# Optimization experiments

Hardware: AMD Instinct MI355X
Metric: run time of the kernel (lower is better)

The kernel has to match this reference:

```python
import jax, jax.numpy as jnp
import numpy as np
from jax import lax

E = 8          # num_experts
K = 2          # top-k
TASKS = 8
GATE_DIM = 16
# (in, expand, out, kernel, stride) per MoE stage
STAGES = [(3, 32, 16, 7, 2), (16, 64, 32, 3, 1), (32, 128, 64, 3, 2), (64, 256, 64, 3, 1), (64, 128, 32, 3, 1)]
DN = ('NCHW', 'OIHW', 'NCHW')


def _pw(x, w):
    return lax.conv_general_dilated(x, w, (1, 1), 'VALID', dimension_numbers=DN)


def _dw(x, w, s):
    p = w.shape[-1] // 2
    return lax.conv_general_dilated(x, w, (s, s), [(p, p), (p, p)], dimension_numbers=DN, feature_group_count=x.shape[1])


def _gn(x, scale, bias):
    # GroupNorm with num_groups = C // 4, eps = 1e-5 (torch default)
    B, C, H, W = x.shape
    G = C // 4
    xr = x.reshape(B, G, -1)
    m = xr.mean(-1, keepdims=True)
    v = xr.var(-1, keepdims=True)
    xn = ((xr - m) * lax.rsqrt(v + 1e-5)).reshape(B, C, H, W)
    return xn * scale[None, :, None, None] + bias[None, :, None, None]


def _dsc(x, p, stride):
    # DSCBlock: pw-conv -> GN -> SiLU -> dw-conv -> GN -> SiLU -> pw-conv -> GN
    w1, s1, b1, w2, s2, b2, w3, s3, b3 = p
    x = jax.nn.silu(_gn(_pw(x, w1), s1, b1))
    x = jax.nn.silu(_gn(_dw(x, w2, stride), s2, b2))
    return _gn(_pw(x, w3), s3, b3)


def _moe(gate_input, x, wg, p, stride, task_bh):
    # task-conditioned top-k softmax gating (noisy_gating=False, all aux loss weights 0)
    logits = gate_input @ wg[task_bh]                      # (B, E)
    probs = jax.nn.softmax(logits, axis=-1)
    topv, topi = lax.top_k(probs, K)
    topv = topv / topv.sum(-1, keepdims=True)              # renormalize top-k gates
    Bn = gate_input.shape[0]
    dense = jnp.zeros_like(probs).at[jnp.arange(Bn)[:, None], topi].set(topv)
    eo = jax.vmap(lambda pe: _dsc(x, pe, stride))(p)       # (E, B, C, H, W)
    return jnp.einsum('be,ebchw->bchw', dense, eo)


def _forward(fl, task_bh):
    gi, xi, ppe = fl[0], fl[1], fl[2]
    x = xi
    for i, (_, _, _, _, s) in enumerate(STAGES):
        base = 3 + i * 10
        wg = fl[base]
        p = tuple(fl[base + 1: base + 10])
        x = _moe(gi, x, wg, p, s, task_bh)
    Bn = x.shape[0]
    # patchify: (B,32,20,20) -> unfold(2,4,4).unfold(3,4,4) -> permute -> (B,25,512)
    patches = x.reshape(Bn, 32, 5, 4, 5, 4).transpose(0, 1, 2, 4, 3, 5)  # (B,32,5,5,4,4)
    patches = patches.transpose(0, 2, 3, 4, 5, 1).reshape(Bn, 25, 512)
    return patches + ppe


def setup_inputs():
    key = jax.random.key(0)
    ks = iter(jax.random.split(key, 256))
    B = 64
    d = {}
    d['gate_input'] = jax.random.normal(next(ks), (B, GATE_DIM), jnp.float32)
    d['expert_input'] = jax.random.normal(next(ks), (B, 3, 80, 80), jnp.float32)
    d['patch_pos_embed'] = 0.02 * jax.random.normal(next(ks), (1, 25, 512), jnp.float32)
    for i, (cin, exp, cout, k, s) in enumerate(STAGES, 1):
        d[f's{i}_wg'] = 0.1 * jax.random.normal(next(ks), (TASKS, GATE_DIM, E), jnp.float32)
        d[f's{i}_w1'] = jax.random.normal(next(ks), (E, exp, cin, 1, 1), jnp.float32) / np.sqrt(cin)
        d[f's{i}_g1s'] = 1.0 + 0.1 * jax.random.normal(next(ks), (E, exp), jnp.float32)
        d[f's{i}_g1b'] = 0.1 * jax.random.normal(next(ks), (E, exp), jnp.float32)
        d[f's{i}_w2'] = jax.random.normal(next(ks), (E, exp, 1, k, k), jnp.float32) / k
        d[f's{i}_g2s'] = 1.0 + 0.1 * jax.random.normal(next(ks), (E, exp), jnp.float32)
        d[f's{i}_g2b'] = 0.1 * jax.random.normal(next(ks), (E, exp), jnp.float32)
        d[f's{i}_w3'] = jax.random.normal(next(ks), (E, cout, exp, 1, 1), jnp.float32) / np.sqrt(exp)
        d[f's{i}_g3s'] = 1.0 + 0.1 * jax.random.normal(next(ks), (E, cout), jnp.float32)
        d[f's{i}_g3b'] = 0.1 * jax.random.normal(next(ks), (E, cout), jnp.float32)
    d['task_bh'] = 3
    return d


def reference(gate_input, expert_input, patch_pos_embed, s1_wg, s1_w1, s1_g1s, s1_g1b, s1_w2, s1_g2s, s1_g2b, s1_w3, s1_g3s, s1_g3b, s2_wg, s2_w1, s2_g1s, s2_g1b, s2_w2, s2_g2s, s2_g2b, s2_w3, s2_g3s, s2_g3b, s3_wg, s3_w1, s3_g1s, s3_g1b, s3_w2, s3_g2s, s3_g2b, s3_w3, s3_g3s, s3_g3b, s4_wg, s4_w1, s4_g1s, s4_g1b, s4_w2, s4_g2s, s4_g2b, s4_w3, s4_g3s, s4_g3b, s5_wg, s5_w1, s5_g1s, s5_g1b, s5_w2, s5_g2s, s5_g2b, s5_w3, s5_g3s, s5_g3b, task_bh):
    fl = (gate_input, expert_input, patch_pos_embed,
          s1_wg, s1_w1, s1_g1s, s1_g1b, s1_w2, s1_g2s, s1_g2b, s1_w3, s1_g3s, s1_g3b,
          s2_wg, s2_w1, s2_g1s, s2_g1b, s2_w2, s2_g2s, s2_g2b, s2_w3, s2_g3s, s2_g3b,
          s3_wg, s3_w1, s3_g1s, s3_g1b, s3_w2, s3_g2s, s3_g2b, s3_w3, s3_g3s, s3_g3b,
          s4_wg, s4_w1, s4_g1s, s4_g1b, s4_w2, s4_g2s, s4_g2b, s4_w3, s4_g3s, s4_g3b,
          s5_wg, s5_w1, s5_g1s, s5_g1b, s5_w2, s5_g2s, s5_g2b, s5_w3, s5_g3s, s5_g3b)
    patches = _forward(fl, task_bh)
    loss = jnp.zeros((), patches.dtype)  # all MoE loss weights are 0 in VisionEncoder
    return (patches, loss)
```

## Files before the change

### kernel.cpp

```cpp
#include <hip/hip_runtime.h>
#include <cstddef>

#define TPB 256

typedef __attribute__((ext_vector_type(8))) short short8v;
typedef __attribute__((ext_vector_type(4))) float f32x4;

__device__ __forceinline__ int rfl(int v) { return __builtin_amdgcn_readfirstlane(v); }
__device__ __forceinline__ float rflf(float v) {
    return __int_as_float(__builtin_amdgcn_readfirstlane(__float_as_int(v)));
}

__device__ __forceinline__ unsigned short f2bf(float f) {
    union { float f; unsigned int u; } x{f};
    unsigned int r = x.u + 0x7fffu + ((x.u >> 16) & 1u);
    return (unsigned short)(r >> 16);
}
__device__ __forceinline__ float bf2f(unsigned short u) {
    return __uint_as_float(((unsigned int)u) << 16);
}

template <int N, int NW>
__device__ __forceinline__ void bredN(float* v, float* red) {
    __syncthreads();
// ... 35 lines not shown
    const int task = taskp[0];
    const float* wg = gp.wg[s] + (size_t)task * 16 * 8;
    float l[8];
    #pragma unroll
    for (int e = 0; e < 8; e++) l[e] = 0.f;
    for (int d = 0; d < 16; d++) {
        float v = gi[b * 16 + d];
        #pragma unroll
        for (int e = 0; e < 8; e++) l[e] += v * wg[d * 8 + e];
    }
    float mx = l[0];
    #pragma unroll
    for (int e = 1; e < 8; e++) mx = fmaxf(mx, l[e]);
    float p[8]; float sum = 0.f;
    #pragma unroll
    for (int e = 0; e < 8; e++) { p[e] = expf(l[e] - mx); sum += p[e]; }
    int i0 = 0;
    #pragma unroll
    for (int e = 1; e < 8; e++) if (p[e] > p[i0]) i0 = e;
    int i1 = (i0 == 0) ? 1 : 0;
    #pragma unroll
    for (int e = 0; e < 8; e++) if (e != i0 && p[e] > p[i1]) i1 = e;
    const float denom = p[i0] + p[i1];
    const int base = (s * 64 + b) * 2;
    gidx[base] = i0; gidx[base + 1] = i1;
    gw[base] = p[i0] / denom; gw[base + 1] = p[i1] / denom;
}

template <int M, int K, int N, int MT, int NCHK, bool FOLD, bool BIN>
__global__ __launch_bounds__(256) void gemm_bf16(
    const unsigned short* __restrict__ inp, const float* __restrict__ wmat,
    const int* __restrict__ gidx, const float* __restrict__ foldStats,
    const float* __restrict__ foldS, const float* __restrict__ foldB,
    unsigned short* __restrict__ outp, float* __restrict__ stats) {
    constexpr int KITERS = (K + 31) / 32;
    constexpr int IM = (MT == 64) ? 2 : 1;
    constexpr int IN = (MT == 16) ? 1 : 2;
    const int bx = blockIdx.x;
    const int nc = bx % NCHK, mc = bx / NCHK;
    const int b = blockIdx.y, slot = blockIdx.z;
    const int bs = b * 2 + slot;
    const int e = rfl(gidx[b * 2 + slot]);
    const int n0 = nc * 64, m0 = mc * MT;
    const int tid = threadIdx.x;
    const int lane = tid & 63, wv = tid >> 6;
    const int quad = lane >> 4, l15 = lane & 15;

    __shared__ __align__(16) unsigned short wtile[MT * 40];
    __shared__ unsigned int intile[16 * 65];
    __shared__ float sred[(MT / 4) * 2];
    __shared__ float afv[K], bfv[K];

    if (tid < (MT / 4) * 2) sred[tid] = 0.f;
    if constexpr (FOLD) {
        for (int c = tid; c < K; c += 256) {
            const int g = c >> 2;
            const float s1 = foldStats[((size_t)bs * (K / 4) + g) * 2 + 0];
            const float s2 = foldStats[((size_t)bs * (K / 4) + g) * 2 + 1];
            const float mean = s1 / (4.f * N);
            const float var = s2 / (4.f * N) - mean * mean;
            const float inv = rsqrtf(var + 1e-5f);
            const float sc = foldS[e * K + c], bi = foldB[e * K + c];
            afv[c] = inv * sc;
            bfv[c] = bi - mean * inv * sc;
        }
    }

    int mbase, nbase;
    if constexpr (MT == 64) { mbase = (wv & 1) * 32; nbase = (wv >> 1) * 32; }
    else if constexpr (MT == 32) { mbase = (wv & 1) * 16; nbase = (wv >> 1) * 32; }
    else { mbase = 0; nbase = wv * 16; }

    f32x4 acc[IM][IN];
    #pragma unroll
    for (int im = 0; im < IM; im++)
        #pragma unroll
        for (int in = 0; in < IN; in++)
            #pragma unroll
            for (int r = 0; r < 4; r++) acc[im][in][r] = 0.f;

    const unsigned short* ib = inp + (size_t)(BIN ? b : bs) * K * N;
    const float* wbase = wmat + (size_t)e * M * K;

    for (int k0 = 0; k0 < KITERS * 32; k0 += 32) {
        __syncthreads();
        for (int i = tid; i < MT * 32; i += 256) {
            const int m = i >> 5, kk = i & 31;
            const float v = (k0 + kk < K) ? wbase[(size_t)(m0 + m) * K + k0 + kk] : 0.f;
            wtile[m * 40 + kk] = f2bf(v);
        }
        {
            const int kp = tid >> 4, nq = tid & 15;
            const int k = k0 + kp * 2;
            const int n = n0 + nq * 4;
            unsigned short u0[4] = {0, 0, 0, 0}, u1[4] = {0, 0, 0, 0};
            const bool nv = (n < N);
            if (nv && k < K) {
                const ushort4 t = *(const ushort4*)(ib + (size_t)k * N + n);
                u0[0] = t.x; u0[1] = t.y; u0[2] = t.z; u0[3] = t.w;
            }
            if (nv && k + 1 < K) {
                const ushort4 t = *(const ushort4*)(ib + (size_t)(k + 1) * N + n);
                u1[0] = t.x; u1[1] = t.y; u1[2] = t.z; u1[3] = t.w;
            }
            #pragma unroll
            for (int t = 0; t < 4; t++) {
                float f0, f1;
                if constexpr (FOLD) {
                    f0 = (nv && k < K) ? silu_f(afv[k] * bf2f(u0[t]) + bfv[k]) : 0.f;
                    f1 = (nv && k + 1 < K) ? silu_f(afv[k + 1] * bf2f(u1[t]) + bfv[k + 1]) : 0.f;
                } else {
                    f0 = bf2f(u0[t]); f1 = bf2f(u1[t]);
                }
                intile[kp * 65 + nq * 4 + t] =
                    (unsigned int)f2bf(f0) | ((unsigned int)f2bf(f1) << 16);
            }
        }
        __syncthreads();

        short8v afr[IM];
        #pragma unroll
        for (int im = 0; im < IM; im++) {
            const int m = mbase + im * 16 + l15;
            afr[im] = *(const short8v*)&wtile[m * 40 + quad * 8];
        }
        #pragma unroll
        for (int in = 0; in < IN; in++) {
            union { unsigned int u[4]; short8v s; } bu;
            const int col = nbase + in * 16 + l15;
            #pragma unroll
            for (int i = 0; i < 4; i++) bu.u[i] = intile[(quad * 4 + i) * 65 + col];
            #pragma unroll
            for (int im = 0; im < IM; im++)
                acc[im][in] = __builtin_amdgcn_mfma_f32_16x16x32_bf16(
                    afr[im], bu.s, acc[im][in], 0, 0, 0);
        }
    }

    unsigned short* ob = outp + (size_t)bs * M * N;
    #pragma unroll
    for (int im = 0; im < IM; im++) {
        #pragma unroll
        for (int in = 0; in < IN; in++) {
            const int n = n0 + nbase + in * 16 + l15;
            float s1 = 0.f, s2 = 0.f;
            #pragma unroll
            for (int r = 0; r < 4; r++) {
                const float a = acc[im][in][r];
                s1 += a; s2 += a * a;
            }
            if (n < N) {
                #pragma unroll
                for (int r = 0; r < 4; r++) {
                    const int m = m0 + mbase + im * 16 + quad * 4 + r;
                    ob[(size_t)m * N + n] = f2bf(acc[im][in][r]);
                }
            }
            #pragma unroll
            for (int off = 8; off > 0; off >>= 1) {
                s1 += __shfl_down(s1, off, 16);
                s2 += __shfl_down(s2, off, 16);
            }
            if (l15 == 0) {
                const int gl = (mbase + im * 16) / 4 + quad;
                atomicAdd(&sred[gl * 2 + 0], s1);
                atomicAdd(&sred[gl * 2 + 1], s2);
            }
        }
    }
    __syncthreads();
    for (int i = tid; i < MT / 4; i += 256) {
        float* sp = stats + (((size_t)bs * (M / 4) + mc * (MT / 4) + i) * NCHK + nc) * 2;
        sp[0] = sred[i * 2]; sp[1] = sred[i * 2 + 1];
    }
}

template <int CEXP, int H, int W, int NCH, int TPBk, int NCHK1>
__global__ __launch_bounds__(TPBk) void dw_k(
    const unsigned short* __restrict__ raw1, const float* __restrict__ stats1,
    const float* __restrict__ g1s, const float* __restrict__ g1b,
    const float* __restrict__ w2, const int* __restrict__ gidx,
    unsigned short* __restrict__ act2raw, float* __restrict__ stats2) {
    constexpr int HW = H * W, HP = H + 2, WPL = W + 3;
    constexpr int NPV = HW / 4, NG = NCH / 4, NW = TPBk / 64;
    constexpr int Qc = HW / 4, QT = NCH * Qc, QI = (QT + TPBk - 1) / TPBk;
    constexpr int G1 = CEXP / 4;
    const int gch = blockIdx.x, b = blockIdx.y, slot = blockIdx.z;
    const int bs = b * 2 + slot;
    const int tid = threadIdx.x;
    const int e = rfl(gidx[b * 2 + slot]);
    const int cb0 = gch * NCH;

    __shared__ float buf1[NCH * HP * WPL];
    __shared__ float w2s[NCH * 9];
    __shared__ float afl[NCH], bfl[NCH];
    __shared__ float red[2 * NG * NW];

    for (int i = tid; i < NCH * HP * WPL; i += TPBk) buf1[i] = 0.f;
    if (tid < NCH * 9) w2s[tid] = w2[((size_t)e * CEXP + cb0) * 9 + tid];
    if (tid < NCH) {
        const int c = cb0 + tid, g = c >> 2;
        float s1 = 0.f, s2 = 0.f;
        for (int i = 0; i < NCHK1; i++) {
            s1 += stats1[(((size_t)bs * G1 + g) * NCHK1 + i) * 2 + 0];
            s2 += stats1[(((size_t)bs * G1 + g) * NCHK1 + i) * 2 + 1];
        }
        const float mean = s1 / (4.f * HW);
        const float var = s2 / (4.f * HW) - mean * mean;
        const float inv = rsqrtf(var + 1e-5f);
        const float sc = g1s[e * CEXP + c], bi = g1b[e * CEXP + c];
        afl[tid] = inv * sc; bfl[tid] = bi - mean * inv * sc;
    }
    __syncthreads();

    const unsigned short* rb = raw1 + (size_t)bs * CEXP * HW + (size_t)cb0 * HW;
    for (int i = tid; i < NCH * NPV; i += TPBk) {
        const int c = i / NPV, pv = i - c * NPV;
        const int p4 = pv * 4, ph = p4 / W, pwb = p4 - ph * W;
        const ushort4 u = *(const ushort4*)(rb + (size_t)c * HW + p4);
        const float a = afl[c], bb = bfl[c];
        float* bp = &buf1[(c * HP + ph + 1) * WPL + pwb + 1];
        bp[0] = silu_f(a * bf2f(u.x) + bb);
        bp[1] = silu_f(a * bf2f(u.y) + bb);
        bp[2] = silu_f(a * bf2f(u.z) + bb);
        bp[3] = silu_f(a * bf2f(u.w) + bb);
    }
    __syncthreads();

    float st2[2 * NG];
    #pragma unroll
    for (int i = 0; i < 2 * NG; i++) st2[i] = 0.f;
    unsigned short* ao = act2raw + (size_t)bs * CEXP * HW + (size_t)cb0 * HW;
    #pragma unroll
    for (int qi = 0; qi < QI; qi++) {
        const int q = tid + qi * TPBk;
        if (QI * TPBk == QT || q < QT) {
            const int c = q / Qc, qq = q - c * Qc;
            const int oh = qq % H, owb = (qq / H) * 4;
            float o[4] = {0.f, 0.f, 0.f, 0.f};
            #pragma unroll
            for (int kh = 0; kh < 3; kh++) {
                const int base = (c * HP + oh + kh) * WPL + owb;
                float r[6];
                #pragma unroll
                for (int i = 0; i < 6; i++) r[i] = buf1[base + i];
                const float wa = w2s[c * 9 + kh * 3 + 0];
                const float wb = w2s[c * 9 + kh * 3 + 1];
                const float wcc = w2s[c * 9 + kh * 3 + 2];
                #pragma unroll
                for (int t = 0; t < 4; t++)
                    o[t] += wa * r[t] + wb * r[t + 1] + wcc * r[t + 2];
            }
            ushort4 ov = {f2bf(o[0]), f2bf(o[1]), f2bf(o[2]), f2bf(o[3])};
            *(ushort4*)(ao + c * HW + oh * W + owb) = ov;
            #pragma unroll
            for (int t = 0; t < 4; t++) {
                if constexpr (NG == 1) { st2[0] += o[t]; st2[1] += o[t] * o[t]; }
                else {
                    const bool gs = (c >= 4);
                    float a0 = gs ? 0.f : o[t], a1 = gs ? o[t] : 0.f;
                    st2[0] += a0; st2[1] += a0 * a0;
                    st2[2] += a1; st2[3] += a1 * a1;
                }
            }
        }
    }
    bredN<2 * NG, NW>(st2, red);
    if (tid == 0) {
        #pragma unroll
        for (int g = 0; g < NG; g++) {
            stats2[((size_t)bs * G1 + cb0 / 4 + g) * 2 + 0] = st2[g * 2];
            stats2[((size_t)bs * G1 + cb0 / 4 + g) * 2 + 1] = st2[g * 2 + 1];
        }
    }
}

__global__ __launch_bounds__(256) void s1_stats(
    const float* __restrict__ xin, const float* __restrict__ w1,
    const int* __restrict__ gidx, float* __restrict__ stats1) {
    const int g = blockIdx.x, b = blockIdx.y, slot = blockIdx.z;
    const int tid = threadIdx.x;
    const int e = rfl(gidx[b * 2 + slot]);
    __shared__ float red[8];
    const float* xb = xin + (size_t)b * 3 * 6400;
    const float* w1e = w1 + ((size_t)e * 32 + g * 4) * 3;
    float wr[4][3];
    #pragma unroll
    for (int c = 0; c < 4; c++)
        #pragma unroll
        for (int k = 0; k < 3; k++) wr[c][k] = rflf(w1e[c * 3 + k]);
    float s[2] = {0.f, 0.f};
    #pragma unroll
    for (int j = 0; j < 7; j++) {
        const int i = j * 256 + tid;
        if (i < 1600) {
            const int p4 = i * 4;
            const float4 v0 = *(const float4*)(xb + p4);
            const float4 v1 = *(const float4*)(xb + 6400 + p4);
            const float4 v2 = *(const float4*)(xb + 12800 + p4);
            const float a0[4] = {v0.x, v0.y, v0.z, v0.w};
            const float a1[4] = {v1.x, v1.y, v1.z, v1.w};
            const float a2[4] = {v2.x, v2.y, v2.z, v2.w};
            #pragma unroll
            for (int t = 0; t < 4; t++)
                #pragma unroll
// ... 130 lines not shown
    const float* __restrict__ g2s, const float* __restrict__ g2b,
    const int* __restrict__ gidx, unsigned short* __restrict__ act2) {
    const int g = blockIdx.x, b = blockIdx.y, slot = blockIdx.z;
    const int tid = threadIdx.x;
    const int e = rfl(gidx[b * 2 + slot]);
    const float* sp = stats2 + ((size_t)(b * 2 + slot) * 8 + g) * 8;
    const float s1 = rflf(sp[0]) + rflf(sp[2]) + rflf(sp[4]) + rflf(sp[6]);
    const float s2 = rflf(sp[1]) + rflf(sp[3]) + rflf(sp[5]) + rflf(sp[7]);
    const float mean2 = s1 / 6400.f;
    const float var2 = s2 / 6400.f - mean2 * mean2;
    const float inv2 = rsqrtf(var2 + 1e-5f);
    const float* rb = rawdw + (size_t)(b * 2 + slot) * 32 * 1600 + (size_t)g * 4 * 1600;
    unsigned short* ao = act2 + ((size_t)(b * 2 + slot) * 32 + g * 4) * 1600;
    #pragma unroll
    for (int c = 0; c < 4; c++) {
        const float sc = rflf(g2s[e * 32 + g * 4 + c]);
        const float bi = rflf(g2b[e * 32 + g * 4 + c]);
        #pragma unroll
        for (int qi = 0; qi < 2; qi++) {
            const int i = tid + qi * 256;
            if (i < 400) {
                const float4 v = *(const float4*)(rb + c * 1600 + i * 4);
                ushort4 ov;
                ov.x = f2bf(silu_f((v.x - mean2) * inv2 * sc + bi));
                ov.y = f2bf(silu_f((v.y - mean2) * inv2 * sc + bi));
                ov.z = f2bf(silu_f((v.z - mean2) * inv2 * sc + bi));
                ov.w = f2bf(silu_f((v.w - mean2) * inv2 * sc + bi));
                *(ushort4*)(ao + c * 1600 + i * 4) = ov;
            }
        }
    }
}

template <int CIN, int CEXP, int KS, int STRIDE, int H, int W, int HO, int WO,
          int NCH, int TPBk>
__global__ __launch_bounds__(TPBk) void dsc_ab_v2(
    const unsigned short* __restrict__ xin, const float* __restrict__ w1,
    const float* __restrict__ g1s, const float* __restrict__ g1b,
    const float* __restrict__ w2,
    const float* __restrict__ g2s, const float* __restrict__ g2b,
    const int* __restrict__ gidx, unsigned short* __restrict__ act2) {
    constexpr int HW = H * W, HWO = HO * WO;
    constexpr int HP = H + 2, WPL = W + 3, EVW = (W + 2) / 2;
    constexpr int NPV = HW / 4;
    constexpr int JN = (NPV + TPBk - 1) / TPBk;
    constexpr int NW = TPBk / 64;
    constexpr int NG = NCH / 4;
    constexpr int Qc = HWO / 4;
    constexpr int QT = NCH * Qc;
    constexpr int QI = (QT + TPBk - 1) / TPBk;
    constexpr int KK = KS * KS;
    const int gch = blockIdx.x, b = blockIdx.y, slot = blockIdx.z;
    const int tid = threadIdx.x;
    const int e = rfl(gidx[b * 2 + slot]);
    const int cb0 = gch * NCH;

    __shared__ float buf1[NCH * HP * WPL];
    __shared__ float w2s[NCH * KK];
    __shared__ float sc2s[NCH], bi2s[NCH];
    __shared__ float red[2 * NG * NW];

    for (int i = tid; i < NCH * HP * WPL; i += TPBk) buf1[i] = 0.f;
    for (int i = tid; i < NCH * KK; i += TPBk) {
        int c = i / KK, k = i - c * KK;
        w2s[i] = w2[((size_t)e * CEXP + cb0 + c) * KK + k];
    }
    if (tid < NCH) {
        sc2s[tid] = g2s[e * CEXP + cb0 + tid];
        bi2s[tid] = g2b[e * CEXP + cb0 + tid];
    }

    const unsigned short* xb = xin + (size_t)b * CIN * HW;
    const float* w1e = w1 + ((size_t)e * CEXP + cb0) * CIN;

    float acc[NCH][JN][4];
    #pragma unroll
    for (int c = 0; c < NCH; c++)
        #pragma unroll
        for (int j = 0; j < JN; j++)
            #pragma unroll
            for (int t = 0; t < 4; t++) acc[c][j][t] = 0.f;

    for (int cb = 0; cb < CIN; cb += 4) {
        float wr[NCH][4];
        #pragma unroll
        for (int c = 0; c < NCH; c++)
            #pragma unroll
            for (int k = 0; k < 4; k++) wr[c][k] = rflf(w1e[c * CIN + cb + k]);
        #pragma unroll
        for (int j = 0; j < JN; j++) {
            const int pv = tid + j * TPBk;
            if (JN * TPBk == NPV || pv < NPV) {
                #pragma unroll
                for (int k = 0; k < 4; k++) {
                    const ushort4 v4 = *(const ushort4*)(xb + (cb + k) * HW + pv * 4);
                    const float va[4] = {bf2f(v4.x), bf2f(v4.y), bf2f(v4.z), bf2f(v4.w)};
                    #pragma unroll
                    for (int c = 0; c < NCH; c++)
                        #pragma unroll
                        for (int t = 0; t < 4; t++)
                            acc[c][j][t] = fmaf(wr[c][k], va[t], acc[c][j][t]);
                }
            }
        }
    }
    float st[2 * NG];
    #pragma unroll
    for (int i = 0; i < 2 * NG; i++) st[i] = 0.f;
    #pragma unroll
    for (int c = 0; c < NCH; c++) {
        const int gs = (c >> 2) * 2;
        #pragma unroll
        for (int j = 0; j < JN; j++)
            #pragma unroll
            for (int t = 0; t < 4; t++) {
                float a = acc[c][j][t];
                st[gs] += a; st[gs + 1] += a * a;
            }
    }
    bredN<2 * NG, NW>(st, red);
    float mg[NG], ig[NG];
    #pragma unroll
    for (int g = 0; g < NG; g++) {
        mg[g] = st[g * 2] / (4.f * HW);
        float var = st[g * 2 + 1] / (4.f * HW) - mg[g] * mg[g];
        ig[g] = rsqrtf(var + 1e-5f);
    }
    float sc1r[NCH], bi1r[NCH];
    #pragma unroll
    for (int c = 0; c < NCH; c++) {
        sc1r[c] = rflf(g1s[e * CEXP + cb0 + c]);
        bi1r[c] = rflf(g1b[e * CEXP + cb0 + c]);
    }
    #pragma unroll
    for (int j = 0; j < JN; j++) {
        const int pv = tid + j * TPBk;
        if (JN * TPBk == NPV || pv < NPV) {
            const int p4 = pv * 4;
            const int ph = p4 / W, pwb = p4 - ph * W;
            #pragma unroll
            for (int c = 0; c < NCH; c++) {
                const int g = (NG == 1) ? 0 : (c >> 2);
                #pragma unroll
                for (int t = 0; t < 4; t++) {
                    float v = silu_f((acc[c][j][t] - mg[g]) * ig[g] * sc1r[c] + bi1r[c]);
                    const int j2 = pwb + t + 1;
                    const int col = (STRIDE == 1) ? j2
                                    : ((j2 & 1) ? EVW + (j2 >> 1) : (j2 >> 1));
                    buf1[(c * HP + ph + 1) * WPL + col] = v;
                }
            }
        }
    }
    __syncthreads();

    float dacc[QI][4];
    float st2[2 * NG];
    #pragma unroll
    for (int i = 0; i < 2 * NG; i++) st2[i] = 0.f;
    #pragma unroll
    for (int qi = 0; qi < QI; qi++) {
        #pragma unroll
        for (int t = 0; t < 4; t++) dacc[qi][t] = 0.f;
        const int q = tid + qi * TPBk;
        if (QI * TPBk == QT || q < QT) {
            const int c = q / Qc, qq = q - c * Qc;
            const int oh = qq % HO, owb = (qq / HO) * 4;
            float o[4] = {0.f, 0.f, 0.f, 0.f};
            if (STRIDE == 1) {
                #pragma unroll
                for (int kh = 0; kh < KS; kh++) {
                    const int base = (c * HP + oh + kh) * WPL + owb;
                    float r[6];
                    #pragma unroll
                    for (int i = 0; i < 6; i++) r[i] = buf1[base + i];
                    const float wa = w2s[c * KK + kh * KS + 0];
                    const float wb = w2s[c * KK + kh * KS + 1];
                    const float wcc = w2s[c * KK + kh * KS + 2];
                    #pragma unroll
                    for (int t = 0; t < 4; t++)
                        o[t] += wa * r[t] + wb * r[t + 1] + wcc * r[t + 2];
                }
            } else {
                #pragma unroll
                for (int kh = 0; kh < KS; kh++) {
                    const int base = (c * HP + 2 * oh + kh) * WPL;
                    float ev[5], od[4];
                    #pragma unroll
                    for (int i = 0; i < 5; i++) ev[i] = buf1[base + owb + i];
                    #pragma unroll
                    for (int i = 0; i < 4; i++) od[i] = buf1[base + EVW + owb + i];
                    const float wa = w2s[c * KK + kh * KS + 0];
                    const float wb = w2s[c * KK + kh * KS + 1];
                    const float wcc = w2s[c * KK + kh * KS + 2];
                    #pragma unroll
                    for (int t = 0; t < 4; t++)
                        o[t] += wa * ev[t] + wb * od[t] + wcc * ev[t + 1];
                }
            }
            #pragma unroll
            for (int t = 0; t < 4; t++) {
                float a = o[t];
                dacc[qi][t] = a;
                if constexpr (NG == 1) {
                    st2[0] += a; st2[1] += a * a;
                } else {
                    const bool gsel = (c >= 4);
                    float a0 = gsel ? 0.f : a, a1 = gsel ? a : 0.f;
                    st2[0] += a0; st2[1] += a0 * a0;
                    st2[2] += a1; st2[3] += a1 * a1;
                }
            }
        }
    }
    bredN<2 * NG, NW>(st2, red);
    float m2[NG], i2[NG];
    #pragma unroll
    for (int g = 0; g < NG; g++) {
        m2[g] = st2[g * 2] / (4.f * HWO);
        float var = st2[g * 2 + 1] / (4.f * HWO) - m2[g] * m2[g];
        i2[g] = rsqrtf(var + 1e-5f);
    }
    unsigned short* ao = act2 + ((size_t)(b * 2 + slot) * CEXP + cb0) * HWO;
    #pragma unroll
    for (int qi = 0; qi < QI; qi++) {
        const int q = tid + qi * TPBk;
        if (QI * TPBk == QT || q < QT) {
            const int c = q / Qc, qq = q - c * Qc;
            const int oh = qq % HO, owb = (qq / HO) * 4;
            const int g = (NG == 1) ? 0 : ((c >= 4) ? 1 : 0);
            const float sc = sc2s[c], bi = bi2s[c];
            ushort4 ov;
            ov.x = f2bf(silu_f((dacc[qi][0] - m2[g]) * i2[g] * sc + bi));
            ov.y = f2bf(silu_f((dacc[qi][1] - m2[g]) * i2[g] * sc + bi));
            ov.z = f2bf(silu_f((dacc[qi][2] - m2[g]) * i2[g] * sc + bi));
            ov.w = f2bf(silu_f((dacc[qi][3] - m2[g]) * i2[g] * sc + bi));
            *(ushort4*)(ao + c * HWO + oh * WO + owb) = ov;
        }
    }
}

template <int COUT, int HWO, int PXC, bool PATCH>
__global__ __launch_bounds__(256) void pw3_k3m(
    const unsigned short* __restrict__ raw3, const float* __restrict__ statsw,
    const float* __restrict__ g3s, const float* __restrict__ g3b,
    const int* __restrict__ gidx, const float* __restrict__ gw,
    const float* __restrict__ ppe, float* __restrict__ outf,
    unsigned short* __restrict__ outb) {
    constexpr int G = COUT / 4;
    constexpr int Q = HWO / 4;
    const int gg = blockIdx.x, b = blockIdx.y;
    const int tid = threadIdx.x;

    float A[2][4], Bv[2][4];
    #pragma unroll
    for (int slot = 0; slot < 2; slot++) {
        const int e = rfl(gidx[b * 2 + slot]);
        const float wgt = rflf(gw[b * 2 + slot]);
        const float* sp = statsw + ((size_t)(b * 2 + slot) * G + gg) * PXC * 2;
        float s1 = 0.f, s2 = 0.f;
        for (int i = 0; i < PXC; i++) { s1 += rflf(sp[i * 2]); s2 += rflf(sp[i * 2 + 1]); }
        const float mean = s1 / (4.f * HWO);
        const float var = s2 / (4.f * HWO) - mean * mean;
        const float inv = rsqrtf(var + 1e-5f);
        #pragma unroll
        for (int i = 0; i < 4; i++) {
            const int c = gg * 4 + i;
            const float sc = rflf(g3s[e * COUT + c]);
            const float bi = rflf(g3b[e * COUT + c]);
            A[slot][i] = wgt * inv * sc;
            Bv[slot][i] = wgt * (bi - mean * inv * sc);
        }
    }

// ... 23 lines not shown
                const float* pp = ppe + p * 512;
                #pragma unroll
                for (int jj = 0; jj < 4; jj++)
                    op[dbase + jj * 32] = o[jj] + pp[dbase + jj * 32];
            }
        }
    }
    if (PATCH && gg == 0 && b == 0 && tid == 0) outf[64 * 25 * 512] = 0.f;
}

extern "C" void kernel_launch(void* const* d_in, const int* in_sizes, int n_in,
                              void* d_out, int out_size, void* d_ws, size_t ws_size,
                              hipStream_t stream) {
    const float* gate_input = (const float*)d_in[0];
    const float* expert_input = (const float*)d_in[1];
    const float* ppe = (const float*)d_in[2];
    const int* taskp = (const int*)d_in[53];
    auto in = [&](int s, int k) { return (const float*)d_in[3 + s * 10 + k]; };

    char* ws = (char*)d_ws;
    int* gidx = (int*)ws;
    float* gw = (float*)(ws + 4096);
    size_t off = 8192;
    unsigned short* x0 = (unsigned short*)(ws + off); off += (size_t)8 << 20;
    unsigned short* x1 = (unsigned short*)(ws + off); off += (size_t)8 << 20;
    unsigned short* act2 = (unsigned short*)(ws + off); off += (size_t)27 << 20;
    char* bufA = ws + off; off += (size_t)27 << 20;
    float* stats1 = (float*)(ws + off); off += (size_t)2 << 20;
    float* stats2 = (float*)(ws + off); off += 262144;
    float* stats3 = (float*)(ws + off); off += (size_t)1 << 20;
    float* st1a = (float*)(ws + off); off += 65536;
    float* st1b = (float*)(ws + off);
    float* outp = (float*)d_out;

    GatePtrs gp;
    for (int s = 0; s < 5; s++) gp.wg[s] = in(s, 0);
    gate_kernel<<<5, 64, 0, stream>>>(gate_input, gp, taskp, gidx, gw);

    s1_stats<<<dim3(8, 64, 2), 256, 0, stream>>>(expert_input, in(0, 1),
                                                 gidx + 0 * 128, st1a);
    s1_band<<<dim3(32, 64, 2), 256, 0, stream>>>(
        expert_input, in(0, 1), in(0, 2), in(0, 3), in(0, 4),
        gidx + 0 * 128, st1a, (float*)bufA, st1b);
    s1_norm<<<dim3(8, 64, 2), 256, 0, stream>>>(
        (float*)bufA, st1b, in(0, 5), in(0, 6), gidx + 0 * 128, act2);
    gemm_bf16<16, 32, 1600, 16, 25, false, false><<<dim3(25, 64, 2), 256, 0, stream>>>(
        act2, in(0, 7), gidx + 0 * 128, nullptr, nullptr, nullptr,
        (unsigned short*)bufA, stats3);
    pw3_k3m<16, 1600, 25, false><<<dim3(4, 64), 256, 0, stream>>>(
        (unsigned short*)bufA, stats3, in(0, 8), in(0, 9), gidx + 0 * 128,
        gw + 0 * 128, ppe, nullptr, x0);

    gemm_bf16<64, 16, 1600, 64, 25, false, true><<<dim3(25, 64, 2), 256, 0, stream>>>(
        x0, in(1, 1), gidx + 1 * 128, nullptr, nullptr, nullptr,
        (unsigned short*)bufA, stats1);
    dw_k<64, 40, 40, 4, 256, 25><<<dim3(16, 64, 2), 256, 0, stream>>>(
        (unsigned short*)bufA, stats1, in(1, 2), in(1, 3), in(1, 4),
        gidx + 1 * 128, act2, stats2);
    gemm_bf16<32, 64, 1600, 32, 25, true, false><<<dim3(25, 64, 2), 256, 0, stream>>>(
        act2, in(1, 7), gidx + 1 * 128, stats2, in(1, 5), in(1, 6),
        (unsigned short*)bufA, stats3);
    pw3_k3m<32, 1600, 25, false><<<dim3(8, 64), 256, 0, stream>>>(
        (unsigned short*)bufA, stats3, in(1, 8), in(1, 9), gidx + 1 * 128,
        gw + 1 * 128, ppe, nullptr, x1);

    dsc_ab_v2<32, 128, 3, 2, 40, 40, 20, 20, 4, 256><<<dim3(32, 64, 2), 256, 0, stream>>>(
        x1, in(2, 1), in(2, 2), in(2, 3), in(2, 4), in(2, 5), in(2, 6),
        gidx + 2 * 128, act2);
    gemm_bf16<64, 128, 400, 64, 7, false, false><<<dim3(7, 64, 2), 256, 0, stream>>>(
        act2, in(2, 7), gidx + 2 * 128, nullptr, nullptr, nullptr,
        (unsigned short*)bufA, stats3);
    pw3_k3m<64, 400, 7, false><<<dim3(16, 64), 256, 0, stream>>>(
        (unsigned short*)bufA, stats3, in(2, 8), in(2, 9), gidx + 2 * 128,
        gw + 2 * 128, ppe, nullptr, x0);

    gemm_bf16<256, 64, 400, 64, 7, false, true><<<dim3(28, 64, 2), 256, 0, stream>>>(
        x0, in(3, 1), gidx + 3 * 128, nullptr, nullptr, nullptr,
        (unsigned short*)bufA, stats1);
    dw_k<256, 20, 20, 8, 128, 7><<<dim3(32, 64, 2), 128, 0, stream>>>(
        (unsigned short*)bufA, stats1, in(3, 2), in(3, 3), in(3, 4),
        gidx + 3 * 128, act2, stats2);
    gemm_bf16<64, 256, 400, 64, 7, true, false><<<dim3(7, 64, 2), 256, 0, stream>>>(
        act2, in(3, 7), gidx + 3 * 128, stats2, in(3, 5), in(3, 6),
        (unsigned short*)bufA, stats3);
    pw3_k3m<64, 400, 7, false><<<dim3(16, 64), 256, 0, stream>>>(
        (unsigned short*)bufA, stats3, in(3, 8), in(3, 9), gidx + 3 * 128,
        gw + 3 * 128, ppe, nullptr, x1);

    gemm_bf16<128, 64, 400, 64, 7, false, true><<<dim3(14, 64, 2), 256, 0, stream>>>(
        x1, in(4, 1), gidx + 4 * 128, nullptr, nullptr, nullptr,
        (unsigned short*)bufA, stats1);
    dw_k<128, 20, 20, 8, 128, 7><<<dim3(16, 64, 2), 128, 0, stream>>>(
        (unsigned short*)bufA, stats1, in(4, 2), in(4, 3), in(4, 4),
        gidx + 4 * 128, act2, stats2);
    gemm_bf16<32, 128, 400, 32, 7, true, false><<<dim3(7, 64, 2), 256, 0, stream>>>(
        act2, in(4, 7), gidx + 4 * 128, stats2, in(4, 5), in(4, 6),
        (unsigned short*)bufA, stats3);
    pw3_k3m<32, 400, 7, true><<<dim3(8, 64), 256, 0, stream>>>(
        (unsigned short*)bufA, stats3, in(4, 8), in(4, 9), gidx + 4 * 128,
        gw + 4 * 128, ppe, outp, nullptr);
}
```

Measured before the change: 523.9 us.

## Split bf16 weights into hi/lo MFMA passes and replace stage-3 fused dsc kernel

Every pointwise GEMM now splits each fp32 weight into a high and a low bf16 part and issues two MFMAs per tile, which doubles matrix work and LDS traffic for weights in exchange for near-fp32 weight precision. The stage-3 fused pointwise+depthwise kernel is removed. It is replaced by two GEMM halves over 64 channels each, followed by a strided depthwise kernel, and the final GEMM now folds the GroupNorm. The dw kernel gains stride and channel-offset support. This looks mainly like an accuracy fix that adds launches and compute.

```diff
diff --git a/kernel.cpp b/kernel.cpp
--- a/kernel.cpp
+++ b/kernel.cpp
@@ -91,7 +91,8 @@
     const unsigned short* __restrict__ inp, const float* __restrict__ wmat,
     const int* __restrict__ gidx, const float* __restrict__ foldStats,
     const float* __restrict__ foldS, const float* __restrict__ foldB,
-    unsigned short* __restrict__ outp, float* __restrict__ stats) {
+    unsigned short* __restrict__ outp, float* __restrict__ stats,
+    int mfull, int moff) {
     constexpr int KITERS = (K + 31) / 32;
     constexpr int IM = (MT == 64) ? 2 : 1;
     constexpr int IN = (MT == 16) ? 1 : 2;
@@ -105,7 +106,8 @@
     const int lane = tid & 63, wv = tid >> 6;
     const int quad = lane >> 4, l15 = lane & 15;
 
-    __shared__ __align__(16) unsigned short wtile[MT * 40];
+    __shared__ __align__(16) unsigned short wtileH[MT * 40];
+    __shared__ __align__(16) unsigned short wtileL[MT * 40];
     __shared__ unsigned int intile[16 * 65];
     __shared__ float sred[(MT / 4) * 2];
     __shared__ float afv[K], bfv[K];
@@ -139,14 +141,16 @@
             for (int r = 0; r < 4; r++) acc[im][in][r] = 0.f;
 
     const unsigned short* ib = inp + (size_t)(BIN ? b : bs) * K * N;
-    const float* wbase = wmat + (size_t)e * M * K;
+    const float* wbase = wmat + ((size_t)e * mfull + moff) * K;
 
     for (int k0 = 0; k0 < KITERS * 32; k0 += 32) {
         __syncthreads();
         for (int i = tid; i < MT * 32; i += 256) {
             const int m = i >> 5, kk = i & 31;
             const float v = (k0 + kk < K) ? wbase[(size_t)(m0 + m) * K + k0 + kk] : 0.f;
-            wtile[m * 40 + kk] = f2bf(v);
+            const unsigned short h = f2bf(v);
+            wtileH[m * 40 + kk] = h;
+            wtileL[m * 40 + kk] = f2bf(v - bf2f(h));
         }
         {
             const int kp = tid >> 4, nq = tid & 15;
@@ -177,11 +181,12 @@
         }
         __syncthreads();
 
-        short8v afr[IM];
+        short8v afrH[IM], afrL[IM];
         #pragma unroll
         for (int im = 0; im < IM; im++) {
             const int m = mbase + im * 16 + l15;
-            afr[im] = *(const short8v*)&wtile[m * 40 + quad * 8];
+            afrH[im] = *(const short8v*)&wtileH[m * 40 + quad * 8];
+            afrL[im] = *(const short8v*)&wtileL[m * 40 + quad * 8];
         }
         #pragma unroll
         for (int in = 0; in < IN; in++) {
@@ -190,9 +195,12 @@
             #pragma unroll
             for (int i = 0; i < 4; i++) bu.u[i] = intile[(quad * 4 + i) * 65 + col];
             #pragma unroll
-            for (int im = 0; im < IM; im++)
+            for (int im = 0; im < IM; im++) {
                 acc[im][in] = __builtin_amdgcn_mfma_f32_16x16x32_bf16(
-                    afr[im], bu.s, acc[im][in], 0, 0, 0);
+                    afrH[im], bu.s, acc[im][in], 0, 0, 0);
+                acc[im][in] = __builtin_amdgcn_mfma_f32_16x16x32_bf16(
+                    afrL[im], bu.s, acc[im][in], 0, 0, 0);
+            }
         }
     }
 
@@ -229,26 +237,29 @@
     }
     __syncthreads();
     for (int i = tid; i < MT / 4; i += 256) {
-        float* sp = stats + (((size_t)bs * (M / 4) + mc * (MT / 4) + i) * NCHK + nc) * 2;
+        float* sp = stats + (((size_t)bs * (mfull / 4) + moff / 4 + mc * (MT / 4) + i)
+                             * NCHK + nc) * 2;
         sp[0] = sred[i * 2]; sp[1] = sred[i * 2 + 1];
     }
 }
 
-template <int CEXP, int H, int W, int NCH, int TPBk, int NCHK1>
+template <int CLOC, int CFULL, int H, int W, int STRIDE, int NCH, int TPBk, int NCHK1>
 __global__ __launch_bounds__(TPBk) void dw_k(
     const unsigned short* __restrict__ raw1, const float* __restrict__ stats1,
     const float* __restrict__ g1s, const float* __restrict__ g1b,
     const float* __restrict__ w2, const int* __restrict__ gidx,
-    unsigned short* __restrict__ act2raw, float* __restrict__ stats2) {
+    unsigned short* __restrict__ act2raw, float* __restrict__ stats2, int coff) {
     constexpr int HW = H * W, HP = H + 2, WPL = W + 3;
+    constexpr int HO = H / STRIDE, WO = W / STRIDE, HWO = HO * WO;
     constexpr int NPV = HW / 4, NG = NCH / 4, NW = TPBk / 64;
-    constexpr int Qc = HW / 4, QT = NCH * Qc, QI = (QT + TPBk - 1) / TPBk;
-    constexpr int G1 = CEXP / 4;
+    constexpr int Qc = HWO / 4, QT = NCH * Qc, QI = (QT + TPBk - 1) / TPBk;
+    constexpr int G1 = CFULL / 4;
     const int gch = blockIdx.x, b = blockIdx.y, slot = blockIdx.z;
     const int bs = b * 2 + slot;
     const int tid = threadIdx.x;
     const int e = rfl(gidx[b * 2 + slot]);
     const int cb0 = gch * NCH;
+    const int cg0 = coff + cb0;
 
     __shared__ float buf1[NCH * HP * WPL];
     __shared__ float w2s[NCH * 9];
@@ -256,9 +267,9 @@
     __shared__ float red[2 * NG * NW];
 
     for (int i = tid; i < NCH * HP * WPL; i += TPBk) buf1[i] = 0.f;
-    if (tid < NCH * 9) w2s[tid] = w2[((size_t)e * CEXP + cb0) * 9 + tid];
+    if (tid < NCH * 9) w2s[tid] = w2[((size_t)e * CFULL + cg0) * 9 + tid];
     if (tid < NCH) {
-        const int c = cb0 + tid, g = c >> 2;
+        const int g = (cg0 + tid) >> 2;
         float s1 = 0.f, s2 = 0.f;
         for (int i = 0; i < NCHK1; i++) {
             s1 += stats1[(((size_t)bs * G1 + g) * NCHK1 + i) * 2 + 0];
@@ -267,12 +278,12 @@
         const float mean = s1 / (4.f * HW);
         const float var = s2 / (4.f * HW) - mean * mean;
         const float inv = rsqrtf(var + 1e-5f);
-        const float sc = g1s[e * CEXP + c], bi = g1b[e * CEXP + c];
+        const float sc = g1s[e * CFULL + cg0 + tid], bi = g1b[e * CFULL + cg0 + tid];
         afl[tid] = inv * sc; bfl[tid] = bi - mean * inv * sc;
     }
     __syncthreads();
 
-    const unsigned short* rb = raw1 + (size_t)bs * CEXP * HW + (size_t)cb0 * HW;
+    const unsigned short* rb = raw1 + (size_t)bs * CLOC * HW + (size_t)cb0 * HW;
     for (int i = tid; i < NCH * NPV; i += TPBk) {
         const int c = i / NPV, pv = i - c * NPV;
         const int p4 = pv * 4, ph = p4 / W, pwb = p4 - ph * W;
@@ -289,29 +300,45 @@
     float st2[2 * NG];
     #pragma unroll
     for (int i = 0; i < 2 * NG; i++) st2[i] = 0.f;
-    unsigned short* ao = act2raw + (size_t)bs * CEXP * HW + (size_t)cb0 * HW;
+    unsigned short* ao = act2raw + (size_t)bs * CFULL * HWO + (size_t)cg0 * HWO;
     #pragma unroll
     for (int qi = 0; qi < QI; qi++) {
         const int q = tid + qi * TPBk;
         if (QI * TPBk == QT || q < QT) {
             const int c = q / Qc, qq = q - c * Qc;
-            const int oh = qq % H, owb = (qq / H) * 4;
+            const int oh = qq % HO, owb = (qq / HO) * 4;
             float o[4] = {0.f, 0.f, 0.f, 0.f};
-            #pragma unroll
-            for (int kh = 0; kh < 3; kh++) {
-                const int base = (c * HP + oh + kh) * WPL + owb;
-                float r[6];
+            if constexpr (STRIDE == 1) {
                 #pragma unroll
-                for (int i = 0; i < 6; i++) r[i] = buf1[base + i];
-                const float wa = w2s[c * 9 + kh * 3 + 0];
-                const float wb = w2s[c * 9 + kh * 3 + 1];
-                const float wcc = w2s[c * 9 + kh * 3 + 2];
+                for (int kh = 0; kh < 3; kh++) {
+                    const int base = (c * HP + oh + kh) * WPL + owb;
+                    float r[6];
+                    #pragma unroll
+                    for (int i = 0; i < 6; i++) r[i] = buf1[base + i];
+                    const float wa = w2s[c * 9 + kh * 3 + 0];
+                    const float wb = w2s[c * 9 + kh * 3 + 1];
+                    const float wcc = w2s[c * 9 + kh * 3 + 2];
+                    #pragma unroll
+                    for (int t = 0; t < 4; t++)
+                        o[t] += wa * r[t] + wb * r[t + 1] + wcc * r[t + 2];
+                }
+            } else {
                 #pragma unroll
-                for (int t = 0; t < 4; t++)
-                    o[t] += wa * r[t] + wb * r[t + 1] + wcc * r[t + 2];
+                for (int kh = 0; kh < 3; kh++) {
+                    const int base = (c * HP + oh * 2 + kh) * WPL + owb * 2;
+                    float r[9];
+                    #pragma unroll
+                    for (int i = 0; i < 9; i++) r[i] = buf1[base + i];
+                    const float wa = w2s[c * 9 + kh * 3 + 0];
+                    const float wb = w2s[c * 9 + kh * 3 + 1];
+                    const float wcc = w2s[c * 9 + kh * 3 + 2];
+                    #pragma unroll
+                    for (int t = 0; t < 4; t++)
+                        o[t] += wa * r[2 * t] + wb * r[2 * t + 1] + wcc * r[2 * t + 2];
+                }
             }
             ushort4 ov = {f2bf(o[0]), f2bf(o[1]), f2bf(o[2]), f2bf(o[3])};
-            *(ushort4*)(ao + c * HW + oh * W + owb) = ov;
+            *(ushort4*)(ao + c * HWO + oh * WO + owb) = ov;
             #pragma unroll
             for (int t = 0; t < 4; t++) {
                 if constexpr (NG == 1) { st2[0] += o[t]; st2[1] += o[t] * o[t]; }
@@ -328,8 +355,8 @@
     if (tid == 0) {
         #pragma unroll
         for (int g = 0; g < NG; g++) {
-            stats2[((size_t)bs * G1 + cb0 / 4 + g) * 2 + 0] = st2[g * 2];
-            stats2[((size_t)bs * G1 + cb0 / 4 + g) * 2 + 1] = st2[g * 2 + 1];
+            stats2[((size_t)bs * G1 + cg0 / 4 + g) * 2 + 0] = st2[g * 2];
+            stats2[((size_t)bs * G1 + cg0 / 4 + g) * 2 + 1] = st2[g * 2 + 1];
         }
     }
 }
@@ -526,214 +553,6 @@
     }
 }
 
-template <int CIN, int CEXP, int KS, int STRIDE, int H, int W, int HO, int WO,
-          int NCH, int TPBk>
-__global__ __launch_bounds__(TPBk) void dsc_ab_v2(
-    const unsigned short* __restrict__ xin, const float* __restrict__ w1,
-    const float* __restrict__ g1s, const float* __restrict__ g1b,
-    const float* __restrict__ w2,
-    const float* __restrict__ g2s, const float* __restrict__ g2b,
-    const int* __restrict__ gidx, unsigned short* __restrict__ act2) {
-    constexpr int HW = H * W, HWO = HO * WO;
-    constexpr int HP = H + 2, WPL = W + 3, EVW = (W + 2) / 2;
-    constexpr int NPV = HW / 4;
-    constexpr int JN = (NPV + TPBk - 1) / TPBk;
-    constexpr int NW = TPBk / 64;
-    constexpr int NG = NCH / 4;
-    constexpr int Qc = HWO / 4;
-    constexpr int QT = NCH * Qc;
-    constexpr int QI = (QT + TPBk - 1) / TPBk;
-    constexpr int KK = KS * KS;
-    const int gch = blockIdx.x, b = blockIdx.y, slot = blockIdx.z;
-    const int tid = threadIdx.x;
-    const int e = rfl(gidx[b * 2 + slot]);
-    const int cb0 = gch * NCH;
-
-    __shared__ float buf1[NCH * HP * WPL];
-    __shared__ float w2s[NCH * KK];
-    __shared__ float sc2s[NCH], bi2s[NCH];
-    __shared__ float red[2 * NG * NW];
-
-    for (int i = tid; i < NCH * HP * WPL; i += TPBk) buf1[i] = 0.f;
-    for (int i = tid; i < NCH * KK; i += TPBk) {
-        int c = i / KK, k = i - c * KK;
-        w2s[i] = w2[((size_t)e * CEXP + cb0 + c) * KK + k];
-    }
-    if (tid < NCH) {
-        sc2s[tid] = g2s[e * CEXP + cb0 + tid];
-        bi2s[tid] = g2b[e * CEXP + cb0 + tid];
-    }
-
-    const unsigned short* xb = xin + (size_t)b * CIN * HW;
-    const float* w1e = w1 + ((size_t)e * CEXP + cb0) * CIN;
-
-    float acc[NCH][JN][4];
-    #pragma unroll
-    for (int c = 0; c < NCH; c++)
-        #pragma unroll
-        for (int j = 0; j < JN; j++)
-            #pragma unroll
-            for (int t = 0; t < 4; t++) acc[c][j][t] = 0.f;
-
-    for (int cb = 0; cb < CIN; cb += 4) {
-        float wr[NCH][4];
-        #pragma unroll
-        for (int c = 0; c < NCH; c++)
-            #pragma unroll
-            for (int k = 0; k < 4; k++) wr[c][k] = rflf(w1e[c * CIN + cb + k]);
-        #pragma unroll
-        for (int j = 0; j < JN; j++) {
-            const int pv = tid + j * TPBk;
-            if (JN * TPBk == NPV || pv < NPV) {
-                #pragma unroll
-                for (int k = 0; k < 4; k++) {
-                    const ushort4 v4 = *(const ushort4*)(xb + (cb + k) * HW + pv * 4);
-                    const float va[4] = {bf2f(v4.x), bf2f(v4.y), bf2f(v4.z), bf2f(v4.w)};
-                    #pragma unroll
-                    for (int c = 0; c < NCH; c++)
-                        #pragma unroll
-                        for (int t = 0; t < 4; t++)
-                            acc[c][j][t] = fmaf(wr[c][k], va[t], acc[c][j][t]);
-                }
-            }
-        }
-    }
-    float st[2 * NG];
-    #pragma unroll
-    for (int i = 0; i < 2 * NG; i++) st[i] = 0.f;
-    #pragma unroll
-    for (int c = 0; c < NCH; c++) {
-        const int gs = (c >> 2) * 2;
-        #pragma unroll
-        for (int j = 0; j < JN; j++)
-            #pragma unroll
-            for (int t = 0; t < 4; t++) {
-                float a = acc[c][j][t];
-                st[gs] += a; st[gs + 1] += a * a;
-            }
-    }
-    bredN<2 * NG, NW>(st, red);
-    float mg[NG], ig[NG];
-    #pragma unroll
-    for (int g = 0; g < NG; g++) {
-        mg[g] = st[g * 2] / (4.f * HW);
-        float var = st[g * 2 + 1] / (4.f * HW) - mg[g] * mg[g];
-        ig[g] = rsqrtf(var + 1e-5f);
-    }
-    float sc1r[NCH], bi1r[NCH];
-    #pragma unroll
-    for (int c = 0; c < NCH; c++) {
-        sc1r[c] = rflf(g1s[e * CEXP + cb0 + c]);
-        bi1r[c] = rflf(g1b[e * CEXP + cb0 + c]);
-    }
-    #pragma unroll
-    for (int j = 0; j < JN; j++) {
-        const int pv = tid + j * TPBk;
-        if (JN * TPBk == NPV || pv < NPV) {
-            const int p4 = pv * 4;
-            const int ph = p4 / W, pwb = p4 - ph * W;
-            #pragma unroll
-            for (int c = 0; c < NCH; c++) {
-                const int g = (NG == 1) ? 0 : (c >> 2);
-                #pragma unroll
-                for (int t = 0; t < 4; t++) {
-                    float v = silu_f((acc[c][j][t] - mg[g]) * ig[g] * sc1r[c] + bi1r[c]);
-                    const int j2 = pwb + t + 1;
-                    const int col = (STRIDE == 1) ? j2
-                                    : ((j2 & 1) ? EVW + (j2 >> 1) : (j2 >> 1));
-                    buf1[(c * HP + ph + 1) * WPL + col] = v;
-                }
-            }
-        }
-    }
-    __syncthreads();
-
-    float dacc[QI][4];
-    float st2[2 * NG];
-    #pragma unroll
-    for (int i = 0; i < 2 * NG; i++) st2[i] = 0.f;
-    #pragma unroll
-    for (int qi = 0; qi < QI; qi++) {
-        #pragma unroll
-        for (int t = 0; t < 4; t++) dacc[qi][t] = 0.f;
-        const int q = tid + qi * TPBk;
-        if (QI * TPBk == QT || q < QT) {
-            const int c = q / Qc, qq = q - c * Qc;
-            const int oh = qq % HO, owb = (qq / HO) * 4;
-            float o[4] = {0.f, 0.f, 0.f, 0.f};
-            if (STRIDE == 1) {
-                #pragma unroll
-                for (int kh = 0; kh < KS; kh++) {
-                    const int base = (c * HP + oh + kh) * WPL + owb;
-                    float r[6];
-                    #pragma unroll
-                    for (int i = 0; i < 6; i++) r[i] = buf1[base + i];
-                    const float wa = w2s[c * KK + kh * KS + 0];
-                    const float wb = w2s[c * KK + kh * KS + 1];
-                    const float wcc = w2s[c * KK + kh * KS + 2];
-                    #pragma unroll
-                    for (int t = 0; t < 4; t++)
-                        o[t] += wa * r[t] + wb * r[t + 1] + wcc * r[t + 2];
-                }
-            } else {
-                #pragma unroll
-                for (int kh = 0; kh < KS; kh++) {
-                    const int base = (c * HP + 2 * oh + kh) * WPL;
-                    float ev[5], od[4];
-                    #pragma unroll
-                    for (int i = 0; i < 5; i++) ev[i] = buf1[base + owb + i];
-                    #pragma unroll
-                    for (int i = 0; i < 4; i++) od[i] = buf1[base + EVW + owb + i];
-                    const float wa = w2s[c * KK + kh * KS + 0];
-                    const float wb = w2s[c * KK + kh * KS + 1];
-                    const float wcc = w2s[c * KK + kh * KS + 2];
-                    #pragma unroll
-                    for (int t = 0; t < 4; t++)
-                        o[t] += wa * ev[t] + wb * od[t] + wcc * ev[t + 1];
-                }
-            }
-            #pragma unroll
-            for (int t = 0; t < 4; t++) {
-                float a = o[t];
-                dacc[qi][t] = a;
-                if constexpr (NG == 1) {
-                    st2[0] += a; st2[1] += a * a;
-                } else {
-                    const bool gsel = (c >= 4);
-                    float a0 = gsel ? 0.f : a, a1 = gsel ? a : 0.f;
-                    st2[0] += a0; st2[1] += a0 * a0;
-                    st2[2] += a1; st2[3] += a1 * a1;
-                }
-            }
-        }
-    }
-    bredN<2 * NG, NW>(st2, red);
-    float m2[NG], i2[NG];
-    #pragma unroll
-    for (int g = 0; g < NG; g++) {
-        m2[g] = st2[g * 2] / (4.f * HWO);
-        float var = st2[g * 2 + 1] / (4.f * HWO) - m2[g] * m2[g];
-        i2[g] = rsqrtf(var + 1e-5f);
-    }
-    unsigned short* ao = act2 + ((size_t)(b * 2 + slot) * CEXP + cb0) * HWO;
-    #pragma unroll
-    for (int qi = 0; qi < QI; qi++) {
-        const int q = tid + qi * TPBk;
-        if (QI * TPBk == QT || q < QT) {
-            const int c = q / Qc, qq = q - c * Qc;
-            const int oh = qq % HO, owb = (qq / HO) * 4;
-            const int g = (NG == 1) ? 0 : ((c >= 4) ? 1 : 0);
-            const float sc = sc2s[c], bi = bi2s[c];
-            ushort4 ov;
-            ov.x = f2bf(silu_f((dacc[qi][0] - m2[g]) * i2[g] * sc + bi));
-            ov.y = f2bf(silu_f((dacc[qi][1] - m2[g]) * i2[g] * sc + bi));
-            ov.z = f2bf(silu_f((dacc[qi][2] - m2[g]) * i2[g] * sc + bi));
-            ov.w = f2bf(silu_f((dacc[qi][3] - m2[g]) * i2[g] * sc + bi));
-            *(ushort4*)(ao + c * HWO + oh * WO + owb) = ov;
-        }
-    }
-}
-
 template <int COUT, int HWO, int PXC, bool PATCH>
 __global__ __launch_bounds__(256) void pw3_k3m(
     const unsigned short* __restrict__ raw3, const float* __restrict__ statsw,
@@ -823,6 +642,7 @@
     float* st1a = (float*)(ws + off); off += 65536;
     float* st1b = (float*)(ws + off);
     float* outp = (float*)d_out;
+    unsigned short* bufA16 = (unsigned short*)bufA;
 
     GatePtrs gp;
     for (int s = 0; s < 5; s++) gp.wg[s] = in(s, 0);
@@ -837,57 +657,66 @@
         (float*)bufA, st1b, in(0, 5), in(0, 6), gidx + 0 * 128, act2);
     gemm_bf16<16, 32, 1600, 16, 25, false, false><<<dim3(25, 64, 2), 256, 0, stream>>>(
         act2, in(0, 7), gidx + 0 * 128, nullptr, nullptr, nullptr,
-        (unsigned short*)bufA, stats3);
+        bufA16, stats3, 16, 0);
     pw3_k3m<16, 1600, 25, false><<<dim3(4, 64), 256, 0, stream>>>(
-        (unsigned short*)bufA, stats3, in(0, 8), in(0, 9), gidx + 0 * 128,
+        bufA16, stats3, in(0, 8), in(0, 9), gidx + 0 * 128,
         gw + 0 * 128, ppe, nullptr, x0);
 
     gemm_bf16<64, 16, 1600, 64, 25, false, true><<<dim3(25, 64, 2), 256, 0, stream>>>(
         x0, in(1, 1), gidx + 1 * 128, nullptr, nullptr, nullptr,
-        (unsigned short*)bufA, stats1);
-    dw_k<64, 40, 40, 4, 256, 25><<<dim3(16, 64, 2), 256, 0, stream>>>(
-        (unsigned short*)bufA, stats1, in(1, 2), in(1, 3), in(1, 4),
-        gidx + 1 * 128, act2, stats2);
+        bufA16, stats1, 64, 0);
+    dw_k<64, 64, 40, 40, 1, 4, 256, 25><<<dim3(16, 64, 2), 256, 0, stream>>>(
+        bufA16, stats1, in(1, 2), in(1, 3), in(1, 4),
+        gidx + 1 * 128, act2, stats2, 0);
     gemm_bf16<32, 64, 1600, 32, 25, true, false><<<dim3(25, 64, 2), 256, 0, stream>>>(
         act2, in(1, 7), gidx + 1 * 128, stats2, in(1, 5), in(1, 6),
-        (unsigned short*)bufA, stats3);
+        bufA16, stats3, 32, 0);
     pw3_k3m<32, 1600, 25, false><<<dim3(8, 64), 256, 0, stream>>>(
-        (unsigned short*)bufA, stats3, in(1, 8), in(1, 9), gidx + 1 * 128,
+        bufA16, stats3, in(1, 8), in(1, 9), gidx + 1 * 128,
         gw + 1 * 128, ppe, nullptr, x1);
 
-    dsc_ab_v2<32, 128, 3, 2, 40, 40, 20, 20, 4, 256><<<dim3(32, 64, 2), 256, 0, stream>>>(
-        x1, in(2, 1), in(2, 2), in(2, 3), in(2, 4), in(2, 5), in(2, 6),
-        gidx + 2 * 128, act2);
-    gemm_bf16<64, 128, 400, 64, 7, false, false><<<dim3(7, 64, 2), 256, 0, stream>>>(
-        act2, in(2, 7), gidx + 2 * 128, nullptr, nullptr, nullptr,
-        (unsigned short*)bufA, stats3);
+    gemm_bf16<64, 32, 1600, 64, 25, false, true><<<dim3(25, 64, 2), 256, 0, stream>>>(
+        x1, in(2, 1), gidx + 2 * 128, nullptr, nullptr, nullptr,
+        bufA16, stats1, 128, 0);
+    dw_k<64, 128, 40, 40, 2, 4, 256, 25><<<dim3(16, 64, 2), 256, 0, stream>>>(
+        bufA16, stats1, in(2, 2), in(2, 3), in(2, 4),
+        gidx + 2 * 128, act2, stats2, 0);
+    gemm_bf16<64, 32, 1600, 64, 25, false, true><<<dim3(25, 64, 2), 256, 0, stream>>>(
+        x1, in(2, 1), gidx + 2 * 128, nullptr, nullptr, nullptr,
+        bufA16, stats1, 128, 64);
+    dw_k<64, 128, 40, 40, 2, 4, 256, 25><<<dim3(16, 64, 2), 256, 0, stream>>>(
+        bufA16, stats1, in(2, 2), in(2, 3), in(2, 4),
+        gidx + 2 * 128, act2, stats2, 64);
+    gemm_bf16<64, 128, 400, 64, 7, true, false><<<dim3(7, 64, 2), 256, 0, stream>>>(
+        act2, in(2, 7), gidx + 2 * 128, stats2, in(2, 5), in(2, 6),
+        bufA16, stats3, 64, 0);
     pw3_k3m<64, 400, 7, false><<<dim3(16, 64), 256, 0, stream>>>(
-        (unsigned short*)bufA, stats3, in(2, 8), in(2, 9), gidx + 2 * 128,
+        bufA16, stats3, in(2, 8), in(2, 9), gidx + 2 * 128,
         gw + 2 * 128, ppe, nullptr, x0);
 
     gemm_bf16<256, 64, 400, 64, 7, false, true><<<dim3(28, 64, 2), 256, 0, stream>>>(
         x0, in(3, 1), gidx + 3 * 128, nullptr, nullptr, nullptr,
-        (unsigned short*)bufA, stats1);
-    dw_k<256, 20, 20, 8, 128, 7><<<dim3(32, 64, 2), 128, 0, stream>>>(
-        (unsigned short*)bufA, stats1, in(3, 2), in(3, 3), in(3, 4),
-        gidx + 3 * 128, act2, stats2);
+        bufA16, stats1, 256, 0);
+    dw_k<256, 256, 20, 20, 1, 8, 128, 7><<<dim3(32, 64, 2), 128, 0, stream>>>(
+        bufA16, stats1, in(3, 2), in(3, 3), in(3, 4),
+        gidx + 3 * 128, act2, stats2, 0);
     gemm_bf16<64, 256, 400, 64, 7, true, false><<<dim3(7, 64, 2), 256, 0, stream>>>(
         act2, in(3, 7), gidx + 3 * 128, stats2, in(3, 5), in(3, 6),
-        (unsigned short*)bufA, stats3);
+        bufA16, stats3, 64, 0);
     pw3_k3m<64, 400, 7, false><<<dim3(16, 64), 256, 0, stream>>>(
-        (unsigned short*)bufA, stats3, in(3, 8), in(3, 9), gidx + 3 * 128,
+        bufA16, stats3, in(3, 8), in(3, 9), gidx + 3 * 128,
         gw + 3 * 128, ppe, nullptr, x1);
 
     gemm_bf16<128, 64, 400, 64, 7, false, true><<<dim3(14, 64, 2), 256, 0, stream>>>(
         x1, in(4, 1), gidx + 4 * 128, nullptr, nullptr, nullptr,
-        (unsigned short*)bufA, stats1);
-    dw_k<128, 20, 20, 8, 128, 7><<<dim3(16, 64, 2), 128, 0, stream>>>(
-        (unsigned short*)bufA, stats1, in(4, 2), in(4, 3), in(4, 4),
-        gidx + 4 * 128, act2, stats2);
+        bufA16, stats1, 128, 0);
+    dw_k<128, 128, 20, 20, 1, 8, 128, 7><<<dim3(16, 64, 2), 128, 0, stream>>>(
+        bufA16, stats1, in(4, 2), in(4, 3), in(4, 4),
+        gidx + 4 * 128, act2, stats2, 0);
     gemm_bf16<32, 128, 400, 32, 7, true, false><<<dim3(7, 64, 2), 256, 0, stream>>>(
         act2, in(4, 7), gidx + 4 * 128, stats2, in(4, 5), in(4, 6),
-        (unsigned short*)bufA, stats3);
+        bufA16, stats3, 32, 0);
     pw3_k3m<32, 400, 7, true><<<dim3(8, 64), 256, 0, stream>>>(
-        (unsigned short*)bufA, stats3, in(4, 8), in(4, 9), gidx + 4 * 128,
+        bufA16, stats3, in(4, 8), in(4, 9), gidx + 4 * 128,
         gw + 4 * 128, ppe, outp, nullptr);
 }
```

New measurement: 551.2 us. +5.2%, slower.
